# Kernel tuning notes

Measured on AMD Instinct MI355X. Metric: run time of the kernel, lower is better.

Reference implementation:

```python
import jax, jax.numpy as jnp
import numpy as np

EPS = 1e-8  # torch F.cosine_similarity denominator clamp
MARGIN = 0.1  # default M in forward signature


def setup_inputs() -> dict:
    key = jax.random.key(0)
    k1, k2 = jax.random.split(key)
    N, B, D = 4096, 1, 1024
    wsi = jax.random.normal(k1, (N, B, D), dtype=jnp.float32)
    omic = jax.random.normal(k2, (N, B, D), dtype=jnp.float32)
    return {"wsi_embeddings": wsi, "omic_embeddings": omic}


def reference(wsi_embeddings, omic_embeddings):
    # [N, B=1, D] -> [N, D]
    W = wsi_embeddings[:, 0, :]
    O = omic_embeddings[:, 0, :]
    nw = jnp.linalg.norm(W, axis=-1)  # [N]
    no = jnp.linalg.norm(O, axis=-1)  # [N]
    # Full pairwise cosine similarity: S[i, j] = cos(wsi_i, omic_j)
    S = (W @ O.T) / jnp.maximum(nw[:, None] * no[None, :], EPS)  # [N, N]
    d = jnp.diagonal(S)  # cos(wsi_i, omic_i), the "self" similarity
    # off-diagonal hinge: relu(M - cos_ij + cos_ii); diagonal: 1 - cos_ii
    off = jax.nn.relu(MARGIN - S + d[:, None])
    eye = jnp.eye(S.shape[0], dtype=bool)
    L = jnp.where(eye, 1.0 - S, off)
    return jnp.mean(L)
```

## Files before the change

kernel.cpp:

```cpp
#include <hip/hip_runtime.h>
#include <stdint.h>

#define N 4096
#define D 1024
#define MARGIN 0.1f
#define BM 256
#define BN 256
#define BKB 128
#define QS 500.0f
#define INVQS2 (1.0f / (QS * QS))

typedef __attribute__((ext_vector_type(4))) int i32x4;

__global__ __launch_bounds__(256) void prep_kernel(
    const float* __restrict__ W, const float* __restrict__ O,
    uint8_t* __restrict__ Wn, uint8_t* __restrict__ On,
    float* __restrict__ dvec, float* __restrict__ out) {
  const int wv = threadIdx.x >> 6, ln = threadIdx.x & 63;
  const int row = blockIdx.x * 4 + wv;
  if (blockIdx.x == 0 && threadIdx.x == 0) *out = 0.0f;
  const float4* Wr = (const float4*)(W + (size_t)row * D);
  const float4* Or = (const float4*)(O + (size_t)row * D);
  float4 w[4], o[4];
  float sw = 0.f, so = 0.f, sd = 0.f;
  #pragma unroll
  for (int c = 0; c < 4; ++c) {
    w[c] = Wr[ln + c * 64];
    o[c] = Or[ln + c * 64];
    sw += w[c].x * w[c].x + w[c].y * w[c].y + w[c].z * w[c].z + w[c].w * w[c].w;
    so += o[c].x * o[c].x + o[c].y * o[c].y + o[c].z * o[c].z + o[c].w * o[c].w;
    sd += w[c].x * o[c].x + w[c].y * o[c].y + w[c].z * o[c].z + w[c].w * o[c].w;
  }
  #pragma unroll
  for (int off = 1; off < 64; off <<= 1) {
    sw += __shfl_xor(sw, off, 64);
    so += __shfl_xor(so, off, 64);
    sd += __shfl_xor(sd, off, 64);
  }
  const float inw = 1.0f / sqrtf(sw) * QS;
  const float ino = 1.0f / sqrtf(so) * QS;
  if (ln == 0) dvec[row] = sd * inw * ino * INVQS2;
  int* Wo = (int*)(Wn + (size_t)row * D);
  int* Oo = (int*)(On + (size_t)row * D);
  #pragma unroll
  for (int c = 0; c < 4; ++c) {
    int q0 = __float2int_rn(fminf(fmaxf(w[c].x * inw, -127.f), 127.f));
    int q1 = __float2int_rn(fminf(fmaxf(w[c].y * inw, -127.f), 127.f));
    int q2 = __float2int_rn(fminf(fmaxf(w[c].z * inw, -127.f), 127.f));
    int q3 = __float2int_rn(fminf(fmaxf(w[c].w * inw, -127.f), 127.f));
    Wo[ln + c * 64] = (q0 & 255) | ((q1 & 255) << 8) | ((q2 & 255) << 16) |
                      ((q3 & 255) << 24);
    q0 = __float2int_rn(fminf(fmaxf(o[c].x * ino, -127.f), 127.f));
    q1 = __float2int_rn(fminf(fmaxf(o[c].y * ino, -127.f), 127.f));
    q2 = __float2int_rn(fminf(fmaxf(o[c].z * ino, -127.f), 127.f));
    q3 = __float2int_rn(fminf(fmaxf(o[c].w * ino, -127.f), 127.f));
    Oo[ln + c * 64] = (q0 & 255) | ((q1 & 255) << 8) | ((q2 & 255) << 16) |
                      ((q3 & 255) << 24);
  }
}

__global__ __launch_bounds__(512) void gemm_loss_kernel(
    const uint8_t* __restrict__ Wn, const uint8_t* __restrict__ On,
    const float* __restrict__ dvec, float* __restrict__ out) {
  __shared__ __align__(16) uint8_t ldsA0[BM * BKB];
  __shared__ __align__(16) uint8_t ldsB0[BN * BKB];
  __shared__ __align__(16) uint8_t ldsA1[BM * BKB];
  __shared__ __align__(16) uint8_t ldsB1[BN * BKB];
  const int bx = blockIdx.x, by = blockIdx.y;
  const int t = threadIdx.x;
  const int wv = t >> 6, ln = t & 63;
  const int wm = wv >> 2, wn = wv & 3;
  const int lrow = ln & 15;
  const int quad = ln >> 4;
  const int l7 = lrow & 7;

  i32x4 acc[8][4] = {};

  const uint8_t* Ag = Wn + (size_t)(by * BM) * D;
  const uint8_t* Bg = On + (size_t)(bx * BN) * D;

#define STAGE(dstA, dstB, ktv) do {                                          \
    _Pragma("unroll")                                                        \
    for (int c_ = 0; c_ < 4; ++c_) {                                         \
      const int g_ = c_ * 512 + t;        \
      const int r_ = g_ >> 3;             \
      const int gi_ = g_ & 7;                   \
      const int col_ = (gi_ ^ (r_ & 7)) << 4;  \
      __builtin_amdgcn_global_load_lds(                                      \
          (const __attribute__((address_space(1))) void*)(                   \
              Ag + (size_t)r_ * D + (ktv) * BKB + col_),                     \
          (__attribute__((address_space(3))) void*)((dstA) + g_ * 16),       \
          16, 0, 0);                                                         \
      __builtin_amdgcn_global_load_lds(                                      \
          (const __attribute__((address_space(1))) void*)(                   \
              Bg + (size_t)r_ * D + (ktv) * BKB + col_),                     \
          (__attribute__((address_space(3))) void*)((dstB) + g_ * 16),       \
          16, 0, 0);                                                         \
    }                                                                        \
  } while (0)

#define COMPUTE(srcA, srcB) do {                                             \
    const int s0a = ((0 * 4 + quad) ^ l7) << 4;        \
    const int s0b = ((1 * 4 + quad) ^ l7) << 4;        \
    i32x4 aF0[8], bF0[4], aF1[8], bF1[4];                                    \
    _Pragma("unroll")                                                        \
    for (int mi = 0; mi < 8; ++mi) {                                         \
      const int rr = wm * 128 + mi * 16 + lrow;                              \
      aF0[mi] = *(const i32x4*)((srcA) + rr * BKB + s0a);                    \
    }                                                                        \
    _Pragma("unroll")                                                        \
    for (int ni = 0; ni < 4; ++ni) {                                         \
      const int cc = wn * 64 + ni * 16 + lrow;                               \
      bF0[ni] = *(const i32x4*)((srcB) + cc * BKB + s0a);                    \
    }                                                                        \
    _Pragma("unroll")                                                        \
    for (int mi = 0; mi < 8; ++mi) {                                         \
      const int rr = wm * 128 + mi * 16 + lrow;                              \
      aF1[mi] = *(const i32x4*)((srcA) + rr * BKB + s0b);                    \
    }                                                                        \
    _Pragma("unroll")                                                        \
    for (int ni = 0; ni < 4; ++ni) {                                         \
      const int cc = wn * 64 + ni * 16 + lrow;                               \
      bF1[ni] = *(const i32x4*)((srcB) + cc * BKB + s0b);                    \
    }                                                                        \
    _Pragma("unroll")                                                        \
    for (int mi = 0; mi < 8; ++mi)                                           \
      _Pragma("unroll")                                                      \
      for (int ni = 0; ni < 4; ++ni)                                         \
        acc[mi][ni] = __builtin_amdgcn_mfma_i32_16x16x64_i8(                 \
            aF0[mi], bF0[ni], acc[mi][ni], 0, 0, 0);                         \
    _Pragma("unroll")                                                        \
    for (int mi = 0; mi < 8; ++mi)                                           \
      _Pragma("unroll")                                                      \
      for (int ni = 0; ni < 4; ++ni)                                         \
        acc[mi][ni] = __builtin_amdgcn_mfma_i32_16x16x64_i8(                 \
            aF1[mi], bF1[ni], acc[mi][ni], 0, 0, 0);                         \
  } while (0)

#define WAITV(n_lit) do {                                                    \
    asm volatile("s_waitcnt vmcnt(" #n_lit ")" ::: "memory");                \
    __builtin_amdgcn_sched_barrier(0);                                       \
  } while (0)
#define BARRIER() do {                                                       \
    __builtin_amdgcn_sched_barrier(0);                                       \
    __builtin_amdgcn_s_barrier();                                            \
    __builtin_amdgcn_sched_barrier(0);                                       \
  } while (0)

  STAGE(ldsA0, ldsB0, 0);
  STAGE(ldsA1, ldsB1, 1); WAITV(8); BARRIER();
  COMPUTE(ldsA0, ldsB0); BARRIER();
  STAGE(ldsA0, ldsB0, 2); WAITV(8); BARRIER();
  COMPUTE(ldsA1, ldsB1); BARRIER();
  STAGE(ldsA1, ldsB1, 3); WAITV(8); BARRIER();
  COMPUTE(ldsA0, ldsB0); BARRIER();
  STAGE(ldsA0, ldsB0, 4); WAITV(8); BARRIER();
  COMPUTE(ldsA1, ldsB1); BARRIER();
  STAGE(ldsA1, ldsB1, 5); WAITV(8); BARRIER();
  COMPUTE(ldsA0, ldsB0); BARRIER();
  STAGE(ldsA0, ldsB0, 6); WAITV(8); BARRIER();
  COMPUTE(ldsA1, ldsB1); BARRIER();
  STAGE(ldsA1, ldsB1, 7); WAITV(8); BARRIER();
  COMPUTE(ldsA0, ldsB0); BARRIER();
  WAITV(0); BARRIER();
  COMPUTE(ldsA1, ldsB1);

  float lsum = 0.0f;
  #pragma unroll
  for (int mi = 0; mi < 8; ++mi) {
    const int gibase = by * BM + wm * 128 + mi * 16 + quad * 4;
    #pragma unroll
    for (int r = 0; r < 4; ++r) {
      const int gi = gibase + r;
      const float di = dvec[gi];
      #pragma unroll
      for (int ni = 0; ni < 4; ++ni) {
        const int gj = bx * BN + wn * 64 + ni * 16 + lrow;
        const float s = (float)acc[mi][ni][r] * INVQS2;
        lsum += (gi == gj) ? (1.0f - s) : fmaxf(MARGIN - s + di, 0.0f);
      }
    }
  }
  #pragma unroll
  for (int off = 32; off; off >>= 1) lsum += __shfl_down(lsum, off, 64);
  __shared__ float bsum[8];
  if (ln == 0) bsum[wv] = lsum;
  __syncthreads();
  if (t == 0) {
    float tot = 0.f;
    #pragma unroll
    for (int i = 0; i < 8; ++i) tot += bsum[i];
    atomicAdd(out, tot * (1.0f / ((float)N * (float)N)));
  }
}

extern "C" void kernel_launch(void* const* d_in, const int* in_sizes, int n_in,
                              void* d_out, int out_size, void* d_ws, size_t ws_size,
                              hipStream_t stream) {
  const float* W = (const float*)d_in[0];
  const float* O = (const float*)d_in[1];
  uint8_t* Wn = (uint8_t*)d_ws;
  uint8_t* On = Wn + (size_t)N * D;
  float* dvec = (float*)(On + (size_t)N * D);
  float* out = (float*)d_out;

  prep_kernel<<<N / 4, 256, 0, stream>>>(W, O, Wn, On, dvec, out);
  dim3 grid(N / BN, N / BM);
  gemm_loss_kernel<<<grid, 512, 0, stream>>>(Wn, On, dvec, out);
}
```

Baseline: 95.50 us.

## Split LDS fragment loads into ping-pong phases with barriers and MFMA priority

Each BKB tile's compute is restructured into k-substeps, and each substep into two half phases that load only part of the A fragments. Barriers and explicit lgkmcnt waits separate LDS reads from MFMA bursts, and s_setprio raises wave priority during MFMA, so waves alternate between memory and math in a ping-pong schedule. This is meant to lower register pressure and let LDS reads of one wave overlap MFMA work of others. In exchange it adds many more workgroup barriers per tile, which can serialise waves.

```diff
diff --git a/kernel.cpp b/kernel.cpp
--- a/kernel.cpp
+++ b/kernel.cpp
@@ -99,71 +99,76 @@
     }                                                                        \
   } while (0)
 
-#define COMPUTE(srcA, srcB) do {                                             \
-    const int s0a = ((0 * 4 + quad) ^ l7) << 4;        \
-    const int s0b = ((1 * 4 + quad) ^ l7) << 4;        \
-    i32x4 aF0[8], bF0[4], aF1[8], bF1[4];                                    \
-    _Pragma("unroll")                                                        \
-    for (int mi = 0; mi < 8; ++mi) {                                         \
-      const int rr = wm * 128 + mi * 16 + lrow;                              \
-      aF0[mi] = *(const i32x4*)((srcA) + rr * BKB + s0a);                    \
-    }                                                                        \
-    _Pragma("unroll")                                                        \
-    for (int ni = 0; ni < 4; ++ni) {                                         \
-      const int cc = wn * 64 + ni * 16 + lrow;                               \
-      bF0[ni] = *(const i32x4*)((srcB) + cc * BKB + s0a);                    \
-    }                                                                        \
-    _Pragma("unroll")                                                        \
-    for (int mi = 0; mi < 8; ++mi) {                                         \
-      const int rr = wm * 128 + mi * 16 + lrow;                              \
-      aF1[mi] = *(const i32x4*)((srcA) + rr * BKB + s0b);                    \
-    }                                                                        \
-    _Pragma("unroll")                                                        \
-    for (int ni = 0; ni < 4; ++ni) {                                         \
-      const int cc = wn * 64 + ni * 16 + lrow;                               \
-      bF1[ni] = *(const i32x4*)((srcB) + cc * BKB + s0b);                    \
-    }                                                                        \
-    _Pragma("unroll")                                                        \
-    for (int mi = 0; mi < 8; ++mi)                                           \
+#define WAITV(n_lit) do {                                                    \
+    asm volatile("s_waitcnt vmcnt(" #n_lit ")" ::: "memory");                \
+    __builtin_amdgcn_sched_barrier(0);                                       \
+  } while (0)
+#define LGKM0() do {                                                         \
+    asm volatile("s_waitcnt lgkmcnt(0)" ::: "memory");                       \
+    __builtin_amdgcn_sched_barrier(0);                                       \
+  } while (0)
+#define BARRIER() do {                                                       \
+    __builtin_amdgcn_sched_barrier(0);                                       \
+    __builtin_amdgcn_s_barrier();                                            \
+    __builtin_amdgcn_sched_barrier(0);                                       \
+  } while (0)
+
+#define KSTEP(srcA, srcB, kkv) do {                                          \
+    const int s0 = (((kkv) * 4 + quad) ^ l7) << 4;                           \
+    i32x4 aL[4], aH[4], bb[4];                                               \
+    _Pragma("unroll")                                                        \
+    for (int mi = 0; mi < 4; ++mi)                                           \
+      aL[mi] = *(const i32x4*)((srcA) + (wm * 128 + mi * 16 + lrow) * BKB + s0); \
+    _Pragma("unroll")                                                        \
+    for (int ni = 0; ni < 4; ++ni)                                           \
+      bb[ni] = *(const i32x4*)((srcB) + (wn * 64 + ni * 16 + lrow) * BKB + s0);  \
+    BARRIER(); LGKM0();                                                      \
+    __builtin_amdgcn_s_setprio(1);                                           \
+    _Pragma("unroll")                                                        \
+    for (int mi = 0; mi < 4; ++mi)                                           \
       _Pragma("unroll")                                                      \
       for (int ni = 0; ni < 4; ++ni)                                         \
         acc[mi][ni] = __builtin_amdgcn_mfma_i32_16x16x64_i8(                 \
-            aF0[mi], bF0[ni], acc[mi][ni], 0, 0, 0);                         \
-    _Pragma("unroll")                                                        \
-    for (int mi = 0; mi < 8; ++mi)                                           \
+            aL[mi], bb[ni], acc[mi][ni], 0, 0, 0);                           \
+    __builtin_amdgcn_s_setprio(0);                                           \
+    BARRIER();                                                               \
+    _Pragma("unroll")                                                        \
+    for (int mi = 0; mi < 4; ++mi)                                           \
+      aH[mi] = *(const i32x4*)((srcA) + (wm * 128 + (mi + 4) * 16 + lrow) * BKB + s0); \
+    BARRIER(); LGKM0();                                                      \
+    __builtin_amdgcn_s_setprio(1);                                           \
+    _Pragma("unroll")                                                        \
+    for (int mi = 0; mi < 4; ++mi)                                           \
       _Pragma("unroll")                                                      \
       for (int ni = 0; ni < 4; ++ni)                                         \
-        acc[mi][ni] = __builtin_amdgcn_mfma_i32_16x16x64_i8(                 \
-            aF1[mi], bF1[ni], acc[mi][ni], 0, 0, 0);                         \
-  } while (0)
-
-#define WAITV(n_lit) do {                                                    \
-    asm volatile("s_waitcnt vmcnt(" #n_lit ")" ::: "memory");                \
-    __builtin_amdgcn_sched_barrier(0);                                       \
-  } while (0)
-#define BARRIER() do {                                                       \
-    __builtin_amdgcn_sched_barrier(0);                                       \
-    __builtin_amdgcn_s_barrier();                                            \
-    __builtin_amdgcn_sched_barrier(0);                                       \
+        acc[mi + 4][ni] = __builtin_amdgcn_mfma_i32_16x16x64_i8(             \
+            aH[mi], bb[ni], acc[mi + 4][ni], 0, 0, 0);                       \
+    __builtin_amdgcn_s_setprio(0);                                           \
+    BARRIER();                                                               \
+  } while (0)
+
+#define PHASES(srcA, srcB) do {                                              \
+    KSTEP(srcA, srcB, 0);                                                    \
+    KSTEP(srcA, srcB, 1);                                                    \
   } while (0)
 
   STAGE(ldsA0, ldsB0, 0);
   STAGE(ldsA1, ldsB1, 1); WAITV(8); BARRIER();
-  COMPUTE(ldsA0, ldsB0); BARRIER();
+  PHASES(ldsA0, ldsB0);
   STAGE(ldsA0, ldsB0, 2); WAITV(8); BARRIER();
-  COMPUTE(ldsA1, ldsB1); BARRIER();
+  PHASES(ldsA1, ldsB1);
   STAGE(ldsA1, ldsB1, 3); WAITV(8); BARRIER();
-  COMPUTE(ldsA0, ldsB0); BARRIER();
+  PHASES(ldsA0, ldsB0);
   STAGE(ldsA0, ldsB0, 4); WAITV(8); BARRIER();
-  COMPUTE(ldsA1, ldsB1); BARRIER();
+  PHASES(ldsA1, ldsB1);
   STAGE(ldsA1, ldsB1, 5); WAITV(8); BARRIER();
-  COMPUTE(ldsA0, ldsB0); BARRIER();
+  PHASES(ldsA0, ldsB0);
   STAGE(ldsA0, ldsB0, 6); WAITV(8); BARRIER();
-  COMPUTE(ldsA1, ldsB1); BARRIER();
+  PHASES(ldsA1, ldsB1);
   STAGE(ldsA1, ldsB1, 7); WAITV(8); BARRIER();
-  COMPUTE(ldsA0, ldsB0); BARRIER();
+  PHASES(ldsA0, ldsB0);
   WAITV(0); BARRIER();
-  COMPUTE(ldsA1, ldsB1);
+  PHASES(ldsA1, ldsB1);
 
   float lsum = 0.0f;
   #pragma unroll
```

New measurement: 97.73 us. +2.3%, slower.
